# Kernel tuning notes

Measured on AMD Instinct MI355X. Metric: run time of the kernel, lower is better.

Reference implementation:

```python
import jax, jax.numpy as jnp
import numpy as np

EMB = 1024
N_HEAD = 16
HEAD = 64
D_FF = 4 * EMB
LN_EPS = 1e-5


def layernorm(x, g, b):
    mu = jnp.mean(x, axis=-1, keepdims=True)
    var = jnp.mean(jnp.square(x - mu), axis=-1, keepdims=True)
    return (x - mu) * jax.lax.rsqrt(var + LN_EPS) * g + b


def setup_inputs() -> dict:
    key = jax.random.key(0)
    ks = jax.random.split(key, 12)
    s = 0.02
    x = jax.random.normal(ks[0], (4, 2048, EMB), dtype=jnp.float32)
    # per-head Q/K/V projections (no bias), stacked along head axis
    Wq = jax.random.normal(ks[1], (N_HEAD, EMB, HEAD), dtype=jnp.float32) * s
    Wk = jax.random.normal(ks[2], (N_HEAD, EMB, HEAD), dtype=jnp.float32) * s
    Wv = jax.random.normal(ks[3], (N_HEAD, EMB, HEAD), dtype=jnp.float32) * s
    Wo = jax.random.normal(ks[4], (EMB, EMB), dtype=jnp.float32) * s
    bo = jnp.zeros((EMB,), dtype=jnp.float32)
    ln1_g = jnp.ones((EMB,), dtype=jnp.float32)
    ln1_b = jnp.zeros((EMB,), dtype=jnp.float32)
    W1 = jax.random.normal(ks[5], (EMB, D_FF), dtype=jnp.float32) * s
    b1 = jnp.zeros((D_FF,), dtype=jnp.float32)
    W2 = jax.random.normal(ks[6], (D_FF, EMB), dtype=jnp.float32) * s
    b2 = jnp.zeros((EMB,), dtype=jnp.float32)
    ln2_g = jnp.ones((EMB,), dtype=jnp.float32)
    ln2_b = jnp.zeros((EMB,), dtype=jnp.float32)
    return dict(x=x, Wq=Wq, Wk=Wk, Wv=Wv, Wo=Wo, bo=bo, ln1_g=ln1_g,
                ln1_b=ln1_b, W1=W1, b1=b1, W2=W2, b2=b2, ln2_g=ln2_g,
                ln2_b=ln2_b)


def reference(x, Wq, Wk, Wv, Wo, bo, ln1_g, ln1_b, W1, b1, W2, b2, ln2_g, ln2_b):
    B, T, _ = x.shape
    # fused multi-head QKV (equivalent to the per-head Python loop + concat)
    q = jnp.einsum('btd,hdk->bhtk', x, Wq)
    k = jnp.einsum('btd,hdk->bhtk', x, Wk)
    v = jnp.einsum('btd,hdk->bhtk', x, Wv)
    scores = jnp.einsum('bhtk,bhsk->bhts', q, k) / jnp.sqrt(jnp.float32(HEAD))
    att = jax.nn.softmax(scores, axis=-1)
    heads = jnp.einsum('bhts,bhsk->bhtk', att, v)           # [B,H,T,head]
    cat = heads.transpose(0, 2, 1, 3).reshape(B, T, EMB)     # concat over heads
    mha = cat @ Wo + bo
    x = x + layernorm(mha, ln1_g, ln1_b)                     # residual of LN(sublayer)
    ff = jax.nn.gelu(x @ W1 + b1, approximate=False) @ W2 + b2
    x = x + layernorm(ff, ln2_g, ln2_b)
    return x
```

## Files before the change

kernel.cpp:

```cpp
#include <hip/hip_runtime.h>
#include <math.h>


using u16 = unsigned short;
typedef __bf16 bf16x8 __attribute__((ext_vector_type(8)));
typedef __bf16 bf16x4 __attribute__((ext_vector_type(4)));
typedef unsigned short u16x8 __attribute__((ext_vector_type(8)));
typedef unsigned short u16x4 __attribute__((ext_vector_type(4)));
typedef float f32x4 __attribute__((ext_vector_type(4)));

#if defined(__has_builtin)
#if __has_builtin(__builtin_amdgcn_exp2f)
#define EXP2F(x) __builtin_amdgcn_exp2f(x)
#endif
#endif
#ifndef EXP2F
#define EXP2F(x) __expf((x) * 0.69314718055994531f)
#endif

__device__ __forceinline__ float bf2f(u16 h) {
  return __uint_as_float(((unsigned int)h) << 16);
}
__device__ __forceinline__ u16 f2bf(float f) {
  unsigned int u = __float_as_uint(f);
  u += 0x7fffu + ((u >> 16) & 1u);
  return (u16)(u >> 16);
}

__device__ __forceinline__ void gload_lds16(const void* g, void* l) {
  __builtin_amdgcn_global_load_lds(
      (__attribute__((address_space(1))) void*)(g),
      (__attribute__((address_space(3))) void*)(l), 16, 0, 0);
}

__global__ __launch_bounds__(256) void detect_dtype(const u16* __restrict__ x,
                                                    int* __restrict__ flag) {
  __shared__ int cnt[256];
  int c = 0;
#pragma unroll
  for (int j = 0; j < 8; ++j) {
    float v = bf2f(x[threadIdx.x * 8 + j]);
    float a = fabsf(v);
    if (a >= 1e-4f && a <= 64.0f) ++c;
  }
  cnt[threadIdx.x] = c;
  __syncthreads();
  if (threadIdx.x == 0) {
    int t = 0;
    for (int i = 0; i < 256; ++i) t += cnt[i];
    flag[0] = (t < 1638) ? 1 : 0;
  }
}

__global__ __launch_bounds__(256) void cvt_copy(const void* __restrict__ in,
                                                u16* __restrict__ out,
                                                const int* __restrict__ flagp,
                                                long n) {
  long idx = ((long)blockIdx.x * 256 + threadIdx.x) * 4;
  if (idx >= n) return;
  if (*flagp) {
    float4 v = *(const float4*)((const float*)in + idx);
    out[idx] = f2bf(v.x); out[idx + 1] = f2bf(v.y);
    out[idx + 2] = f2bf(v.z); out[idx + 3] = f2bf(v.w);
  } else {
    *(u16x4*)(out + idx) = *(const u16x4*)((const u16*)in + idx);
  }
}

__global__ __launch_bounds__(256) void cvt_vecs(
    const void* s0, const void* s1, const void* s2, const void* s3,
    const void* s4, const void* s5, const void* s6, u16* __restrict__ dst,
    const int* __restrict__ flagp) {
  const int lens[7] = {1024, 1024, 1024, 4096, 1024, 1024, 1024};
  const int offs[7] = {0, 1024, 2048, 3072, 7168, 8192, 9216};
  const void* srcs[7] = {s0, s1, s2, s3, s4, s5, s6};
  int w = blockIdx.x;
  int f = *flagp;
  for (int i = threadIdx.x; i < lens[w]; i += 256)
    dst[offs[w] + i] = f ? f2bf(((const float*)srcs[w])[i])
                         : ((const u16*)srcs[w])[i];
}

__global__ __launch_bounds__(256) void transpose_cvt(
    const void* __restrict__ in, u16* __restrict__ out, int R, int C,
    long inBS, long outBS, const int* __restrict__ flagp) {
  __shared__ u16 tile[32][33];
  int f = *flagp;
  u16* ob = out + (long)blockIdx.z * outBS;
  int c = blockIdx.x * 32 + threadIdx.x;
  int r0 = blockIdx.y * 32;
  if (f) {
    const float* ib = (const float*)in + (long)blockIdx.z * inBS;
#pragma unroll
    for (int i = threadIdx.y; i < 32; i += 8)
      tile[i][threadIdx.x] = f2bf(ib[(long)(r0 + i) * C + c]);
  } else {
    const u16* ib = (const u16*)in + (long)blockIdx.z * inBS;
#pragma unroll
    for (int i = threadIdx.y; i < 32; i += 8)
      tile[i][threadIdx.x] = ib[(long)(r0 + i) * C + c];
  }
  __syncthreads();
  int r = r0 + threadIdx.x;
  int c0 = blockIdx.x * 32;
#pragma unroll
  for (int i = threadIdx.y; i < 32; i += 8)
    ob[(long)(c0 + i) * R + r] = tile[threadIdx.x][i];
}

__global__ __launch_bounds__(256) void kv_frag(const u16* __restrict__ qkv,
                                               u16* __restrict__ KF,
                                               u16* __restrict__ VF) {
  __shared__ u16 Kt[64][72];
  __shared__ u16 Vt[64][72];
  const int jblk = blockIdx.x, bh = blockIdx.y;
  const int b = bh >> 4, h = bh & 15;
  const int tid = threadIdx.x;
  const long j0 = jblk * 64;

  {
    int tt = tid >> 2, c0 = (tid & 3) * 16;
    const u16* src = qkv + (long)(b * 2048 + j0 + tt) * 3072 + h * 64 + c0;
    *(u16x8*)(&Kt[tt][c0]) = *(const u16x8*)(src + 1024);
    *(u16x8*)(&Kt[tt][c0 + 8]) = *(const u16x8*)(src + 1024 + 8);
    *(u16x8*)(&Vt[tt][c0]) = *(const u16x8*)(src + 2048);
    *(u16x8*)(&Vt[tt][c0 + 8]) = *(const u16x8*)(src + 2048 + 8);
  }
  __syncthreads();

  long obase = ((long)bh * 32 + jblk) * 8 * 512;
#pragma unroll
  for (int si = 0; si < 2; ++si) {
    int s = tid * 2 + si;
    int f = s >> 6, ln = s & 63;
    int kt = f >> 2, nt = f & 3;
    int lr = ln & 15, lq = ln >> 4;
    u16x8 ko, vo;
#pragma unroll
    for (int j = 0; j < 8; ++j) {
      ko[j] = Kt[nt * 16 + lr][kt * 32 + lq * 8 + j];
      vo[j] = Vt[kt * 32 + lq * 8 + j][nt * 16 + lr];
    }
    *(u16x8*)(KF + obase + (long)s * 8) = ko;
    *(u16x8*)(VF + obase + (long)s * 8) = vo;
  }
}

__device__ __forceinline__ bf16x8 fragld32(const u16* lb, int row, int lq) {
  int slot = lq ^ (row & 3);
  return *(const bf16x8*)(lb + row * 32 + slot * 8);
}

template <int EPI, int BN>
__global__ __launch_bounds__(512, 2) void gemm2ph(
    const u16* __restrict__ A, const u16* __restrict__ Bt,
    const u16* __restrict__ bias, u16* __restrict__ Cout,
    int M, int N, int K) {
  static_assert(BN == 256 || BN == 128, "");
  constexpr int NFQ = BN / 128;
  __shared__ u16 As[2][256 * 32];
  __shared__ u16 Bs[2][BN * 32];
  const int tid = threadIdx.x;
  const int wave = tid >> 6, lane = tid & 63;
  const int lr = lane & 15, lq = lane >> 4;

  const int MT = M >> 8, NTt = N / BN;
  const int nwg = MT * NTt;
  int wg = blockIdx.x;
  if (!(nwg & 7)) wg = (wg & 7) * (nwg >> 3) + (wg >> 3);
  const int tm = wg % MT, tn = wg / MT;
  const long m0 = (long)tm << 8;
  const long n0 = (long)tn * BN;

  const int wm = (wave >> 2) << 7;
  const int wn = (wave & 3) * (BN / 4);

  const int srow = lane >> 2;
  const int skoff = ((lane & 3) ^ (srow & 3)) * 8;

  auto stage = [&](int buf, int t) {
#pragma unroll
    for (int j = 0; j < 2; ++j)
      gload_lds16(
          A + (m0 + j * 128 + wave * 16 + srow) * (long)K + t * 32 + skoff,
          &As[buf][j * 4096 + (wave << 9)]);
#pragma unroll
    for (int j = 0; j < BN / 128; ++j)
      gload_lds16(
          Bt + (n0 + j * 128 + wave * 16 + srow) * (long)K + t * 32 + skoff,
          &Bs[buf][j * 4096 + (wave << 9)]);
  };

  f32x4 acc[8][2 * NFQ] = {};
  const int NT = K >> 5;
  int cur = 0;

  stage(0, 0);
  __syncthreads();

  for (int t = 0; t < NT; ++t) {
    const u16* Ab = As[cur];
    const u16* Bb = Bs[cur];
    if (t + 1 < NT) stage(cur ^ 1, t + 1);

    bf16x8 a_[4], b0_[NFQ], b1_[NFQ];
#pragma unroll
    for (int mf = 0; mf < 4; ++mf) a_[mf] = fragld32(Ab, wm + mf * 16 + lr, lq);
#pragma unroll
    for (int nf = 0; nf < NFQ; ++nf)
      b0_[nf] = fragld32(Bb, wn + nf * 16 + lr, lq);
#pragma unroll
    for (int mf = 0; mf < 4; ++mf)
#pragma unroll
      for (int nf = 0; nf < NFQ; ++nf)
        acc[mf][nf] = __builtin_amdgcn_mfma_f32_16x16x32_bf16(
            a_[mf], b0_[nf], acc[mf][nf], 0, 0, 0);
#pragma unroll
    for (int nf = 0; nf < NFQ; ++nf)
      b1_[nf] = fragld32(Bb, wn + BN / 8 + nf * 16 + lr, lq);
#pragma unroll
    for (int mf = 0; mf < 4; ++mf)
#pragma unroll
      for (int nf = 0; nf < NFQ; ++nf)
        acc[mf][NFQ + nf] = __builtin_amdgcn_mfma_f32_16x16x32_bf16(
            a_[mf], b1_[nf], acc[mf][NFQ + nf], 0, 0, 0);
#pragma unroll
    for (int mf = 0; mf < 4; ++mf)
      a_[mf] = fragld32(Ab, wm + 64 + mf * 16 + lr, lq);
#pragma unroll
    for (int mf = 0; mf < 4; ++mf)
#pragma unroll
      for (int nf = 0; nf < NFQ; ++nf)
        acc[4 + mf][NFQ + nf] = __builtin_amdgcn_mfma_f32_16x16x32_bf16(
            a_[mf], b1_[nf], acc[4 + mf][NFQ + nf], 0, 0, 0);
#pragma unroll
    for (int mf = 0; mf < 4; ++mf)
#pragma unroll
      for (int nf = 0; nf < NFQ; ++nf)
        acc[4 + mf][nf] = __builtin_amdgcn_mfma_f32_16x16x32_bf16(
            a_[mf], b0_[nf], acc[4 + mf][nf], 0, 0, 0);

    __syncthreads();
    cur ^= 1;
  }

  const int rq = lq * 4;
#pragma unroll
  for (int mf = 0; mf < 8; ++mf)
#pragma unroll
    for (int nf2 = 0; nf2 < 2 * NFQ; ++nf2) {
      const int col = (int)n0 + wn + nf2 * 16 + lr;
#pragma unroll
      for (int r = 0; r < 4; ++r) {
        const long row = m0 + wm + mf * 16 + rq + r;
        float v = acc[mf][nf2][r];
        if (EPI == 2) {
          v += bf2f(bias[col]);
          v = 0.5f * v * (1.0f + erff(v * 0.70710678118654752f));
        } else if (EPI == 3) {
          v += bf2f(bias[col]);
        }
        Cout[row * (long)N + col] = f2bf(v);
      }
    }
}

template <int EPI>
__global__ __launch_bounds__(256) void gemm128(
    const u16* __restrict__ A, const u16* __restrict__ Bt,
    const u16* __restrict__ bias, u16* __restrict__ Cout,
    int M, int N, int K) {
  __shared__ u16 As[2][128 * 32];
  __shared__ u16 Bs[2][128 * 32];
  const int tid = threadIdx.x;
  const int wave = tid >> 6, lane = tid & 63;
  const int lr = lane & 15, lq = lane >> 4;

  const int MT = M >> 7, NTt = N >> 7;
  const int nwg = MT * NTt;
  int wg = blockIdx.x;
  if (!(nwg & 7)) wg = (wg & 7) * (nwg >> 3) + (wg >> 3);
  const int tm = wg % MT, tn = wg / MT;
  const long m0 = (long)tm << 7, n0 = (long)tn << 7;
  const int wm = (wave >> 1) * 64, wn = (wave & 1) * 64;

  const int srow = lane >> 2;
  const int skoff = ((lane & 3) ^ (srow & 3)) * 8;

  auto stage = [&](int buf, int t) {
#pragma unroll
    for (int j = 0; j < 2; ++j) {
      gload_lds16(
          A + (m0 + j * 64 + wave * 16 + srow) * (long)K + t * 32 + skoff,
          &As[buf][j * 2048 + (wave << 9)]);
      gload_lds16(
          Bt + (n0 + j * 64 + wave * 16 + srow) * (long)K + t * 32 + skoff,
          &Bs[buf][j * 2048 + (wave << 9)]);
    }
  };

  f32x4 acc[4][4] = {};
  const int NT = K >> 5;
  int cur = 0;

  stage(0, 0);
  __syncthreads();

  for (int t = 0; t < NT; ++t) {
    const u16* Ab = As[cur];
    const u16* Bb = Bs[cur];
    if (t + 1 < NT) stage(cur ^ 1, t + 1);

    bf16x8 a_[4], b_[4];
#pragma unroll
    for (int mf = 0; mf < 4; ++mf) a_[mf] = fragld32(Ab, wm + mf * 16 + lr, lq);
#pragma unroll
    for (int nf = 0; nf < 2; ++nf) b_[nf] = fragld32(Bb, wn + nf * 16 + lr, lq);
#pragma unroll
    for (int mf = 0; mf < 4; ++mf)
#pragma unroll
      for (int nf = 0; nf < 2; ++nf)
        acc[mf][nf] = __builtin_amdgcn_mfma_f32_16x16x32_bf16(
            a_[mf], b_[nf], acc[mf][nf], 0, 0, 0);
#pragma unroll
    for (int nf = 2; nf < 4; ++nf) b_[nf] = fragld32(Bb, wn + nf * 16 + lr, lq);
#pragma unroll
    for (int mf = 0; mf < 4; ++mf)
#pragma unroll
      for (int nf = 2; nf < 4; ++nf)
        acc[mf][nf] = __builtin_amdgcn_mfma_f32_16x16x32_bf16(
            a_[mf], b_[nf], acc[mf][nf], 0, 0, 0);

    __syncthreads();
    cur ^= 1;
  }

  const int rq = lq * 4;
#pragma unroll
  for (int mf = 0; mf < 4; ++mf)
#pragma unroll
    for (int nf = 0; nf < 4; ++nf) {
      const int col = (int)n0 + wn + nf * 16 + lr;
#pragma unroll
      for (int r = 0; r < 4; ++r) {
        const long row = m0 + wm + mf * 16 + rq + r;
        float v = acc[mf][nf][r];
        if (EPI == 2) {
          v += bf2f(bias[col]);
          v = 0.5f * v * (1.0f + erff(v * 0.70710678118654752f));
        } else if (EPI == 3) {
          v += bf2f(bias[col]);
        }
        Cout[row * (long)N + col] = f2bf(v);
      }
    }
}

__global__ __launch_bounds__(256, 3) void flash_attn(
    const u16* __restrict__ qkv, const u16* __restrict__ KF,
    const u16* __restrict__ VF, u16* __restrict__ cat) {
  const int T = 2048, LD = 3072;
  const float QSCALE = 0.18033688011112042f;
  const float EXPC = 4.3280851226677321f;
  const int bh = blockIdx.y;
  const int b = bh >> 4, h = bh & 15;
  const int tid = threadIdx.x, wave = tid >> 6, lane = tid & 63;
  const int lr = lane & 15, lq = lane >> 4;

  __shared__ u16 Ps[4 * 32 * 72];
  u16* Pw = Ps + wave * 32 * 72;

  const u16* Qb = qkv + (long)(b * 2048) * LD + h * 64;
  const long fbase = (long)bh * 32 * 8 * 512;

  bf16x8 aq[2][2];
#pragma unroll
  for (int st = 0; st < 2; ++st) {
    int qrow = blockIdx.x * 128 + wave * 32 + st * 16 + lr;
#pragma unroll
    for (int kt = 0; kt < 2; ++kt) {
      u16x8 q = *(const u16x8*)(Qb + (long)qrow * LD + kt * 32 + lq * 8);
      bf16x8 t;
#pragma unroll
      for (int j = 0; j < 8; ++j) t[j] = (__bf16)(bf2f(q[j]) * QSCALE);
      aq[st][kt] = t;
    }
  }

  f32x4 o[2][4] = {};
  float lsum[2] = {0.0f, 0.0f};

  for (int jblk = 0; jblk < T / 64; ++jblk) {
    const u16* kf = KF + fbase + (long)jblk * 8 * 512;
    const u16* vf = VF + fbase + (long)jblk * 8 * 512;

    bf16x8 bk[2][4];
#pragma unroll
    for (int kt = 0; kt < 2; ++kt)
#pragma unroll
      for (int nt = 0; nt < 4; ++nt)
        bk[kt][nt] = *(const bf16x8*)(kf + (kt * 4 + nt) * 512 + lane * 8);

    f32x4 s[2][4] = {};
    __builtin_amdgcn_s_setprio(1);
#pragma unroll
    for (int st = 0; st < 2; ++st)
#pragma unroll
      for (int nt = 0; nt < 4; ++nt)
#pragma unroll
        for (int kt = 0; kt < 2; ++kt)
          s[st][nt] = __builtin_amdgcn_mfma_f32_16x16x32_bf16(
              bk[kt][nt], aq[st][kt], s[st][nt], 0, 0, 0);
    __builtin_amdgcn_s_setprio(0);

    bf16x8 bv[2][4];
#pragma unroll
    for (int kt = 0; kt < 2; ++kt)
#pragma unroll
      for (int nt = 0; nt < 4; ++nt)
        bv[kt][nt] = *(const bf16x8*)(vf + (kt * 4 + nt) * 512 + lane * 8);

#pragma unroll
    for (int st = 0; st < 2; ++st)
#pragma unroll
      for (int nt = 0; nt < 4; ++nt) {
        f32x4 p;
#pragma unroll
        for (int r = 0; r < 4; ++r) p[r] = EXP2F(s[st][nt][r] - EXPC);
        lsum[st] += (p[0] + p[1]) + (p[2] + p[3]);
        bf16x4 pk;
#pragma unroll
        for (int r = 0; r < 4; ++r) pk[r] = (__bf16)p[r];
        *(bf16x4*)(Pw + (st * 16 + lr) * 72 + nt * 16 + lq * 4) = pk;
      }

#pragma unroll
    for (int st = 0; st < 2; ++st)
#pragma unroll
      for (int kt = 0; kt < 2; ++kt) {
        bf16x8 ap =
            *(const bf16x8*)(Pw + (st * 16 + lr) * 72 + kt * 32 + lq * 8);
        __builtin_amdgcn_s_setprio(1);
#pragma unroll
        for (int nt = 0; nt < 4; ++nt)
          o[st][nt] = __builtin_amdgcn_mfma_f32_16x16x32_bf16(
              ap, bv[kt][nt], o[st][nt], 0, 0, 0);
        __builtin_amdgcn_s_setprio(0);
      }
  }

#pragma unroll
  for (int st = 0; st < 2; ++st) {
    lsum[st] += __shfl_xor(lsum[st], 16, 64);
    lsum[st] += __shfl_xor(lsum[st], 32, 64);
  }

  u16* ob = cat + (long)(b * 2048) * 1024 + h * 64;
#pragma unroll
  for (int st = 0; st < 2; ++st) {
    int trow = blockIdx.x * 128 + wave * 32 + st * 16 + lq * 4;
#pragma unroll
    for (int r = 0; r < 4; ++r) {
      float linv = 1.0f / __shfl(lsum[st], lq * 4 + r, 64);
#pragma unroll
      for (int nt = 0; nt < 4; ++nt)
        ob[(long)(trow + r) * 1024 + nt * 16 + lr] = f2bf(o[st][nt][r] * linv);
    }
  }
}

__global__ __launch_bounds__(256) void ln_residual(
    const u16* __restrict__ y, const void* __restrict__ res, int res_raw,
    const u16* __restrict__ g, const u16* __restrict__ bb,
    void* __restrict__ out, const int* __restrict__ flagp, int final_out) {
  const long row = blockIdx.x;
  const int tid = threadIdx.x, wave = tid >> 6, lane = tid & 63;
  u16x4 yv = *(const u16x4*)(y + row * 1024 + tid * 4);
  float yy[4];
#pragma unroll
  for (int j = 0; j < 4; ++j) yy[j] = bf2f(yv[j]);
  float s1 = yy[0] + yy[1] + yy[2] + yy[3];
  float s2 = yy[0] * yy[0] + yy[1] * yy[1] + yy[2] * yy[2] + yy[3] * yy[3];
#pragma unroll
  for (int off = 1; off < 64; off <<= 1) {
    s1 += __shfl_xor(s1, off, 64);
    s2 += __shfl_xor(s2, off, 64);
  }
  __shared__ float ws1[4], ws2[4];
  if (lane == 0) { ws1[wave] = s1; ws2[wave] = s2; }
  __syncthreads();
  float t1 = ws1[0] + ws1[1] + ws1[2] + ws1[3];
  float t2 = ws2[0] + ws2[1] + ws2[2] + ws2[3];
  float mu = t1 * (1.0f / 1024.0f);
  float var = t2 * (1.0f / 1024.0f) - mu * mu;
  float rstd = rsqrtf(var + 1e-5f);
  int i = tid * 4;
  bool f32in = res_raw && (*flagp);
  bool f32out = final_out && (*flagp);
#pragma unroll
  for (int j = 0; j < 4; ++j) {
    float rv = f32in ? ((const float*)res)[row * 1024 + i + j]
                     : bf2f(((const u16*)res)[row * 1024 + i + j]);
    float o = rv + (yy[j] - mu) * rstd * bf2f(g[i + j]) + bf2f(bb[i + j]);
    if (f32out)
      ((float*)out)[row * 1024 + i + j] = o;
    else
      ((u16*)out)[row * 1024 + i + j] = f2bf(o);
  }
}

extern "C" void kernel_launch(void* const* d_in, const int* in_sizes, int n_in,
                              void* d_out, int out_size, void* d_ws,
                              size_t ws_size, hipStream_t stream) {
  const void* x_raw = d_in[0];
  const void* Wq = d_in[1];
  const void* Wk = d_in[2];
  const void* Wv = d_in[3];
  const void* Wo = d_in[4];
  const void* bo = d_in[5];
  const void* ln1g = d_in[6];
  const void* ln1b = d_in[7];
  const void* W1 = d_in[8];
  const void* b1 = d_in[9];
  const void* W2 = d_in[10];
  const void* b2 = d_in[11];
  const void* ln2g = d_in[12];
  const void* ln2b = d_in[13];

  char* ws = (char*)d_ws;
  u16* qkv = (u16*)(ws + 0);
  u16* mha = (u16*)(ws + 0);
  u16* h1 = (u16*)(ws + 0);
  u16* cat = (u16*)(ws + 50331648);
  u16* KF = (u16*)(ws + 67108864);
  u16* ff = (u16*)(ws + 67108864);
  u16* xb = (u16*)(ws + 83886080);
  u16* VF = (u16*)(ws + 83886080);
  u16* x1 = (u16*)(ws + 83886080);
  u16* wqkvt = (u16*)(ws + 100663296);
  u16* wot = (u16*)(ws + 106954752);
  u16* w1t = (u16*)(ws + 109051904);
  u16* w2t = (u16*)(ws + 117440512);
  u16* vecs = (u16*)(ws + 125829120);
  int* flag = (int*)(ws + 125853696);

  const u16* v_bo = vecs + 0;
  const u16* v_l1g = vecs + 1024;
  const u16* v_l1b = vecs + 2048;
  const u16* v_b1 = vecs + 3072;
  const u16* v_b2 = vecs + 7168;
  const u16* v_l2g = vecs + 8192;
  const u16* v_l2b = vecs + 9216;

  detect_dtype<<<1, 256, 0, stream>>>((const u16*)x_raw, flag);
  cvt_copy<<<8192, 256, 0, stream>>>(x_raw, xb, flag, 8388608L);
  cvt_vecs<<<7, 256, 0, stream>>>(bo, ln1g, ln1b, b1, b2, ln2g, ln2b, vecs, flag);

  dim3 tb(32, 8);
  transpose_cvt<<<dim3(2, 32, 16), tb, 0, stream>>>(Wq, wqkvt, 1024, 64, 65536, 65536, flag);
  transpose_cvt<<<dim3(2, 32, 16), tb, 0, stream>>>(Wk, wqkvt + 1048576, 1024, 64, 65536, 65536, flag);
  transpose_cvt<<<dim3(2, 32, 16), tb, 0, stream>>>(Wv, wqkvt + 2097152, 1024, 64, 65536, 65536, flag);
  transpose_cvt<<<dim3(32, 32, 1), tb, 0, stream>>>(Wo, wot, 1024, 1024, 0, 0, flag);
  transpose_cvt<<<dim3(128, 32, 1), tb, 0, stream>>>(W1, w1t, 1024, 4096, 0, 0, flag);
  transpose_cvt<<<dim3(32, 128, 1), tb, 0, stream>>>(W2, w2t, 4096, 1024, 0, 0, flag);

  gemm2ph<0, 128><<<768, 512, 0, stream>>>(xb, wqkvt, nullptr, qkv, 8192, 3072, 1024);
  kv_frag<<<dim3(32, 64), 256, 0, stream>>>(qkv, KF, VF);
  flash_attn<<<dim3(16, 64), 256, 0, stream>>>(qkv, KF, VF, cat);
  gemm128<3><<<512, 256, 0, stream>>>(cat, wot, v_bo, mha, 8192, 1024, 1024);
  ln_residual<<<8192, 256, 0, stream>>>(mha, x_raw, 1, v_l1g, v_l1b, x1, flag, 0);
  gemm2ph<2, 256><<<512, 512, 0, stream>>>(x1, w1t, v_b1, h1, 8192, 4096, 1024);
  gemm128<3><<<512, 256, 0, stream>>>(h1, w2t, v_b2, ff, 8192, 1024, 4096);
  ln_residual<<<8192, 256, 0, stream>>>(ff, x1, 0, v_l2g, v_l2b, d_out, flag, 1);
}
```

Baseline: 645.4 us.

## Double K-tile depth to 64 in gemm2ph and retune LDS swizzles

The 256-row GEMM kernel now stages 64-wide K slices per iteration instead of 32, with an 8-slot XOR swizzle for the 64-element LDS rows. Each iteration issues twice as many MFMAs, which halves the number of barriers and loop iterations. The gemm128 kernel gets a different swizzle pattern (row>>1) for its 32-wide layout, meant to cut LDS bank conflicts. The cost is doubled LDS use (64KB+ per block with BN=256) and more fragment registers, which could reduce occupancy below the two blocks per CU the launch bounds ask for.

```diff
diff --git a/kernel.cpp b/kernel.cpp
--- a/kernel.cpp
+++ b/kernel.cpp
@@ -146,9 +146,10 @@
   }
 }
 
-__device__ __forceinline__ bf16x8 fragld32(const u16* lb, int row, int lq) {
-  int slot = lq ^ (row & 3);
-  return *(const bf16x8*)(lb + row * 32 + slot * 8);
+__device__ __forceinline__ bf16x8 fragld64(const u16* lb, int row, int ks,
+                                           int lq) {
+  int slot = ((ks << 2) | lq) ^ (row & 7);
+  return *(const bf16x8*)(lb + row * 64 + slot * 8);
 }
 
 template <int EPI, int BN>
@@ -158,8 +159,8 @@
     int M, int N, int K) {
   static_assert(BN == 256 || BN == 128, "");
   constexpr int NFQ = BN / 128;
-  __shared__ u16 As[2][256 * 32];
-  __shared__ u16 Bs[2][BN * 32];
+  __shared__ u16 As[2][16384];
+  __shared__ u16 Bs[2][BN * 64];
   const int tid = threadIdx.x;
   const int wave = tid >> 6, lane = tid & 63;
   const int lr = lane & 15, lq = lane >> 4;
@@ -175,24 +176,24 @@
   const int wm = (wave >> 2) << 7;
   const int wn = (wave & 3) * (BN / 4);
 
-  const int srow = lane >> 2;
-  const int skoff = ((lane & 3) ^ (srow & 3)) * 8;
+  const int srow = lane >> 3;
+  const int skoff = ((lane & 7) ^ srow) * 8;
 
   auto stage = [&](int buf, int t) {
 #pragma unroll
-    for (int j = 0; j < 2; ++j)
+    for (int j = 0; j < 4; ++j)
       gload_lds16(
-          A + (m0 + j * 128 + wave * 16 + srow) * (long)K + t * 32 + skoff,
+          A + (m0 + j * 64 + wave * 8 + srow) * (long)K + t * 64 + skoff,
           &As[buf][j * 4096 + (wave << 9)]);
 #pragma unroll
-    for (int j = 0; j < BN / 128; ++j)
+    for (int j = 0; j < BN / 64; ++j)
       gload_lds16(
-          Bt + (n0 + j * 128 + wave * 16 + srow) * (long)K + t * 32 + skoff,
+          Bt + (n0 + j * 64 + wave * 8 + srow) * (long)K + t * 64 + skoff,
           &Bs[buf][j * 4096 + (wave << 9)]);
   };
 
   f32x4 acc[8][2 * NFQ] = {};
-  const int NT = K >> 5;
+  const int NT = K >> 6;
   int cur = 0;
 
   stage(0, 0);
@@ -203,42 +204,59 @@
     const u16* Bb = Bs[cur];
     if (t + 1 < NT) stage(cur ^ 1, t + 1);
 
-    bf16x8 a_[4], b0_[NFQ], b1_[NFQ];
-#pragma unroll
-    for (int mf = 0; mf < 4; ++mf) a_[mf] = fragld32(Ab, wm + mf * 16 + lr, lq);
+    bf16x8 a_[4][2], b0_[NFQ][2], b1_[NFQ][2];
+#pragma unroll
+    for (int mf = 0; mf < 4; ++mf)
+#pragma unroll
+      for (int ks = 0; ks < 2; ++ks)
+        a_[mf][ks] = fragld64(Ab, wm + mf * 16 + lr, ks, lq);
 #pragma unroll
     for (int nf = 0; nf < NFQ; ++nf)
-      b0_[nf] = fragld32(Bb, wn + nf * 16 + lr, lq);
+#pragma unroll
+      for (int ks = 0; ks < 2; ++ks)
+        b0_[nf][ks] = fragld64(Bb, wn + nf * 16 + lr, ks, lq);
 #pragma unroll
     for (int mf = 0; mf < 4; ++mf)
 #pragma unroll
       for (int nf = 0; nf < NFQ; ++nf)
-        acc[mf][nf] = __builtin_amdgcn_mfma_f32_16x16x32_bf16(
-            a_[mf], b0_[nf], acc[mf][nf], 0, 0, 0);
+#pragma unroll
+        for (int ks = 0; ks < 2; ++ks)
+          acc[mf][nf] = __builtin_amdgcn_mfma_f32_16x16x32_bf16(
+              a_[mf][ks], b0_[nf][ks], acc[mf][nf], 0, 0, 0);
 #pragma unroll
     for (int nf = 0; nf < NFQ; ++nf)
-      b1_[nf] = fragld32(Bb, wn + BN / 8 + nf * 16 + lr, lq);
+#pragma unroll
+      for (int ks = 0; ks < 2; ++ks)
+        b1_[nf][ks] = fragld64(Bb, wn + BN / 8 + nf * 16 + lr, ks, lq);
 #pragma unroll
     for (int mf = 0; mf < 4; ++mf)
 #pragma unroll
       for (int nf = 0; nf < NFQ; ++nf)
-        acc[mf][NFQ + nf] = __builtin_amdgcn_mfma_f32_16x16x32_bf16(
-            a_[mf], b1_[nf], acc[mf][NFQ + nf], 0, 0, 0);
-#pragma unroll
-    for (int mf = 0; mf < 4; ++mf)
-      a_[mf] = fragld32(Ab, wm + 64 + mf * 16 + lr, lq);
+#pragma unroll
+        for (int ks = 0; ks < 2; ++ks)
+          acc[mf][NFQ + nf] = __builtin_amdgcn_mfma_f32_16x16x32_bf16(
+              a_[mf][ks], b1_[nf][ks], acc[mf][NFQ + nf], 0, 0, 0);
+#pragma unroll
+    for (int mf = 0; mf < 4; ++mf)
+#pragma unroll
+      for (int ks = 0; ks < 2; ++ks)
+        a_[mf][ks] = fragld64(Ab, wm + 64 + mf * 16 + lr, ks, lq);
 #pragma unroll
     for (int mf = 0; mf < 4; ++mf)
 #pragma unroll
       for (int nf = 0; nf < NFQ; ++nf)
-        acc[4 + mf][NFQ + nf] = __builtin_amdgcn_mfma_f32_16x16x32_bf16(
-            a_[mf], b1_[nf], acc[4 + mf][NFQ + nf], 0, 0, 0);
+#pragma unroll
+        for (int ks = 0; ks < 2; ++ks)
+          acc[4 + mf][NFQ + nf] = __builtin_amdgcn_mfma_f32_16x16x32_bf16(
+              a_[mf][ks], b1_[nf][ks], acc[4 + mf][NFQ + nf], 0, 0, 0);
 #pragma unroll
     for (int mf = 0; mf < 4; ++mf)
 #pragma unroll
       for (int nf = 0; nf < NFQ; ++nf)
-        acc[4 + mf][nf] = __builtin_amdgcn_mfma_f32_16x16x32_bf16(
-            a_[mf], b0_[nf], acc[4 + mf][nf], 0, 0, 0);
+#pragma unroll
+        for (int ks = 0; ks < 2; ++ks)
+          acc[4 + mf][nf] = __builtin_amdgcn_mfma_f32_16x16x32_bf16(
+              a_[mf][ks], b0_[nf][ks], acc[4 + mf][nf], 0, 0, 0);
 
     __syncthreads();
     cur ^= 1;
@@ -265,6 +283,11 @@
     }
 }
 
+__device__ __forceinline__ bf16x8 fragld32(const u16* lb, int row, int lq) {
+  int slot = lq ^ ((row >> 1) & 3);
+  return *(const bf16x8*)(lb + row * 32 + slot * 8);
+}
+
 template <int EPI>
 __global__ __launch_bounds__(256) void gemm128(
     const u16* __restrict__ A, const u16* __restrict__ Bt,
@@ -285,7 +308,7 @@
   const int wm = (wave >> 1) * 64, wn = (wave & 1) * 64;
 
   const int srow = lane >> 2;
-  const int skoff = ((lane & 3) ^ (srow & 3)) * 8;
+  const int skoff = ((lane & 3) ^ ((lane >> 3) & 3)) * 8;
 
   auto stage = [&](int buf, int t) {
 #pragma unroll
```

Measured after the change: 629.3 us. 2.5% less time.
